# Kernel optimization log

Hardware: AMD Instinct MI355X
Metric: run time of the kernel (lower is better)

Reference implementation:

```python
import jax, jax.numpy as jnp
import numpy as np

EPS = 1e-5
P = 8  # patch size


def ln_chan(x, w, b):
    # LayerNorm over channel dim C of (B,C,H,W): per-pixel mean/var across channels
    mu = x.mean(axis=1, keepdims=True)
    var = x.var(axis=1, keepdims=True)
    return (x - mu) / jnp.sqrt(var + EPS) * w[None, :, None, None] + b[None, :, None, None]


def conv1x1(x, w):
    # w: (O, C) -> pointwise conv
    return jnp.einsum('bchw,oc->bohw', x, w)


def dwconv3(x, w):
    # depthwise 3x3, SAME padding; w: (C,1,3,3)
    return jax.lax.conv_general_dilated(
        x, w, window_strides=(1, 1), padding='SAME',
        dimension_numbers=('NCHW', 'OIHW', 'NCHW'),
        feature_group_count=x.shape[1])


def to_patches(t):
    b, c, h, w = t.shape
    return t.reshape(b, c, h // P, P, w // P, P).transpose(0, 1, 2, 4, 3, 5)


def from_patches(t, h, w):
    b, c = t.shape[:2]
    return t.transpose(0, 1, 2, 4, 3, 5).reshape(b, c, h, w)


def setup_inputs() -> dict:
    key = jax.random.key(0)
    ks = jax.random.split(key, 8)
    B, C, H, W = 4, 64, 256, 256
    s = 0.1  # weight scale to keep activations sane
    inp = {
        'x': jax.random.normal(ks[0], (B, C, H, W), jnp.float32),
        'evt': jax.random.normal(ks[1], (B, C, H, W), jnp.float32),
        'w_q': jax.random.normal(ks[2], (2 * C, C), jnp.float32) * s,
        'w_kv': jax.random.normal(ks[3], (4 * C, C), jnp.float32) * s,
        'w_qdw': jax.random.normal(ks[4], (2 * C, 1, 3, 3), jnp.float32) * s,
        'w_kvdw': jax.random.normal(ks[5], (4 * C, 1, 3, 3), jnp.float32) * s,
        'w_proj': jax.random.normal(ks[6], (C, 2 * C), jnp.float32) * s,
        'ln_img_w': jnp.ones((C,), jnp.float32),
        'ln_img_b': jnp.zeros((C,), jnp.float32),
        'ln_evt_w': jnp.ones((C,), jnp.float32),
        'ln_evt_b': jnp.zeros((C,), jnp.float32),
        'ln_out_w': jnp.ones((2 * C,), jnp.float32),
        'ln_out_b': jnp.zeros((2 * C,), jnp.float32),
    }
    return inp


def reference(x, evt, w_q, w_kv, w_qdw, w_kvdw, w_proj,
              ln_img_w, ln_img_b, ln_evt_w, ln_evt_b, ln_out_w, ln_out_b):
    x = ln_chan(x, ln_img_w, ln_img_b)
    evt = ln_chan(evt, ln_evt_w, ln_evt_b)
    q = dwconv3(conv1x1(x, w_q), w_qdw)          # (B, 2C, H, W)
    kv = dwconv3(conv1x1(evt, w_kv), w_kvdw)     # (B, 4C, H, W)
    k, v = jnp.split(kv, 2, axis=1)
    h, w = q.shape[-2:]
    q_fft = jnp.fft.rfft2(to_patches(q))         # (B,2C,h/8,w/8,8,5) complex
    k_fft = jnp.fft.rfft2(to_patches(k))
    out = jnp.fft.irfft2(q_fft * k_fft, s=(P, P))
    out = from_patches(out, h, w)                # (B, 2C, H, W)
    out = ln_chan(out, ln_out_w, ln_out_b)
    out = v * out
    return conv1x1(out, w_proj)                  # (B, C, H, W)
```

## Files before the change

### kernel.cpp

```cpp
#include <hip/hip_runtime.h>

typedef __attribute__((ext_vector_type(8))) short bf16x8;
typedef __attribute__((ext_vector_type(4))) float f32x4;
typedef __attribute__((ext_vector_type(2))) float f32x2;
typedef __attribute__((ext_vector_type(4))) unsigned int u32x4;
typedef __attribute__((ext_vector_type(2))) unsigned int u32x2;

__device__ __forceinline__ unsigned short f2bf(float f) {
    union { float f; unsigned int u; } v; v.f = f;
    return (unsigned short)((v.u + 0x7fffu + ((v.u >> 16) & 1u)) >> 16);
}
__device__ __forceinline__ float bflo(unsigned int u) {
    union { unsigned int u; float f; } v; v.u = u << 16; return v.f;
}
__device__ __forceinline__ float bfhi(unsigned int u) {
    union { unsigned int u; float f; } v; v.u = u & 0xffff0000u; return v.f;
}
__device__ __forceinline__ f32x2 bfpair(unsigned int u) {
    union { unsigned int u; float f; } lo, hi;
    lo.u = u << 16; hi.u = u & 0xffff0000u;
    return (f32x2){lo.f, hi.f};
}
__device__ __forceinline__ void pkfma(f32x2& d, f32x2 a, f32x2 b) {
    asm("v_pk_fma_f32 %0, %1, %2, %0" : "+v"(d) : "v"(a), "v"(b));
}

__device__ __forceinline__ float wred_allsum(float x) {
    asm volatile(
        "s_nop 1\n\t"
        "v_add_f32_dpp %0, %0, %0 row_shr:1 bound_ctrl:0\n\t"
        "s_nop 1\n\t"
        "v_add_f32_dpp %0, %0, %0 row_shr:2 bound_ctrl:0\n\t"
        "s_nop 1\n\t"
        "v_add_f32_dpp %0, %0, %0 row_shr:4 bound_ctrl:0\n\t"
        "s_nop 1\n\t"
        "v_add_f32_dpp %0, %0, %0 row_shr:8 bound_ctrl:0\n\t"
        "s_nop 1\n\t"
        "v_add_f32_dpp %0, %0, %0 row_bcast:15 row_mask:0xa bound_ctrl:0\n\t"
        "s_nop 1\n\t"
        "v_add_f32_dpp %0, %0, %0 row_bcast:31 row_mask:0xc bound_ctrl:0\n\t"
        "s_nop 1"
        : "+v"(x));
    return __builtin_bit_cast(float, __builtin_amdgcn_readlane(__builtin_bit_cast(int, x), 63));
}

__global__ __launch_bounds__(256, 8)
void ln_kernel(const float* __restrict__ x, const float* __restrict__ evt,
               const float* __restrict__ lwx, const float* __restrict__ lbx,
               const float* __restrict__ lwe, const float* __restrict__ lbe,
               unsigned short* __restrict__ xo, unsigned short* __restrict__ eo)
{
    __shared__ float xt[64][68];
    __shared__ float ps[4][64], ps2[4][64];
    __shared__ float smu[64], sinv[64], slw[64], slb[64];

    const int tid = threadIdx.x;
    const int z = blockIdx.z, b = blockIdx.y;
    const int hw0 = blockIdx.x * 64;
    const float* src = z ? evt : x;
    const float* lw  = z ? lwe : lwx;
    const float* lb  = z ? lbe : lbx;
    unsigned short* dst = z ? eo : xo;

    if (tid < 64) { slw[tid] = lw[tid]; slb[tid] = lb[tid]; }

    const float* sp = src + (size_t)b * 64 * 65536 + hw0;
    #pragma unroll
    for (int it = 0; it < 4; ++it) {
        int i = tid + it * 256;
        int c = i >> 4, p4 = i & 15;
        f32x4 v = *(const f32x4*)&sp[(size_t)c * 65536 + p4 * 4];
        xt[p4 * 4 + 0][c] = v.x;
        xt[p4 * 4 + 1][c] = v.y;
        xt[p4 * 4 + 2][c] = v.z;
        xt[p4 * 4 + 3][c] = v.w;
    }
    __syncthreads();

    {
        int px = tid & 63, part = tid >> 6;
        float s = 0.f, s2 = 0.f;
        #pragma unroll
        for (int j = 0; j < 4; ++j) {
            f32x4 v = *(const f32x4*)&xt[px][part * 16 + j * 4];
            s  += v.x + v.y + v.z + v.w;
            s2 += v.x * v.x + v.y * v.y + v.z * v.z + v.w * v.w;
        }
        ps[part][px] = s; ps2[part][px] = s2;
    }
    __syncthreads();
    if (tid < 64) {
        float s  = ps[0][tid] + ps[1][tid] + ps[2][tid] + ps[3][tid];
        float s2 = ps2[0][tid] + ps2[1][tid] + ps2[2][tid] + ps2[3][tid];
        float mu = s * (1.f / 64.f);
        smu[tid] = mu;
        sinv[tid] = rsqrtf(s2 * (1.f / 64.f) - mu * mu + 1e-5f);
    }
    __syncthreads();

    unsigned short* dp = dst + ((size_t)b * 65536 + hw0) * 64;
    #pragma unroll
    for (int it = 0; it < 2; ++it) {
        int i = tid + it * 256;
        int px = i >> 3, oct = i & 7;
        float mu = smu[px], inv = sinv[px];
        f32x4 v0 = *(const f32x4*)&xt[px][oct * 8];
        f32x4 v1 = *(const f32x4*)&xt[px][oct * 8 + 4];
        u32x4 w;
        int c = oct * 8;
        float a0 = (v0.x - mu) * inv * slw[c + 0] + slb[c + 0];
        float a1 = (v0.y - mu) * inv * slw[c + 1] + slb[c + 1];
        w[0] = (unsigned int)f2bf(a0) | ((unsigned int)f2bf(a1) << 16);
        a0 = (v0.z - mu) * inv * slw[c + 2] + slb[c + 2];
        a1 = (v0.w - mu) * inv * slw[c + 3] + slb[c + 3];
        w[1] = (unsigned int)f2bf(a0) | ((unsigned int)f2bf(a1) << 16);
        a0 = (v1.x - mu) * inv * slw[c + 4] + slb[c + 4];
        a1 = (v1.y - mu) * inv * slw[c + 5] + slb[c + 5];
        w[2] = (unsigned int)f2bf(a0) | ((unsigned int)f2bf(a1) << 16);
        a0 = (v1.z - mu) * inv * slw[c + 6] + slb[c + 6];
        a1 = (v1.w - mu) * inv * slw[c + 7] + slb[c + 7];
        w[3] = (unsigned int)f2bf(a0) | ((unsigned int)f2bf(a1) << 16);
        *(u32x4*)&dp[(size_t)px * 64 + oct * 8] = w;
    }
}

#define PR_WB    14336
#define PR_WDW   30720
#define PR_SMEM  35328

__global__ __launch_bounds__(512, 8)
void prod_kernel(const unsigned short* __restrict__ src,
                 const float* __restrict__ wmat, const float* __restrict__ wdw,
                 unsigned short* __restrict__ dst)
{
    __shared__ __align__(16) char smem[PR_SMEM];
    unsigned short* A   = (unsigned short*)(smem);
    unsigned short* Wb  = (unsigned short*)(smem + PR_WB);
    unsigned short* pre = (unsigned short*)(smem);
    float* swdw = (float*)(smem + PR_WDW);

    const int tid = threadIdx.x;
    const int pj = blockIdx.x, pi = blockIdx.y, b = blockIdx.z;
    const int h0 = pi * 8, w0 = pj * 8;

    #pragma unroll
    for (int it = 0; it < 4; ++it) {
        int i = tid + it * 512;
        int o = i >> 4, c4 = i & 15;
        f32x4 wv = *(const f32x4*)&wmat[o * 64 + c4 * 4];
        unsigned int lo = (unsigned int)f2bf(wv[0]) | ((unsigned int)f2bf(wv[1]) << 16);
        unsigned int hi = (unsigned int)f2bf(wv[2]) | ((unsigned int)f2bf(wv[3]) << 16);
        u32x2 pk = {lo, hi};
        *(u32x2*)&Wb[o * 64 + (((c4 >> 1) ^ (o & 7)) << 3) + (c4 & 1) * 4] = pk;
    }
    for (int i = tid; i < 1152; i += 512) swdw[i] = wdw[i];
    for (int i = tid; i < 768; i += 512) A[6400 + i] = 0;
    #pragma unroll
    for (int it = 0; it < 2; ++it) {
        int i = tid + it * 512;
        if (i < 800) {
            int px = i >> 3, oct = i & 7;
            int r = px / 10, cc = px - r * 10;
            int gh = h0 - 1 + r, gw = w0 - 1 + cc;
            u32x4 val = {0u, 0u, 0u, 0u};
            if (gh >= 0 && gh < 256 && gw >= 0 && gw < 256)
                val = *(const u32x4*)&src[((size_t)(b * 65536 + gh * 256 + gw)) * 64 + oct * 8];
            *(u32x4*)&A[px * 64 + ((oct ^ (px & 7)) << 3)] = val;
        }
    }
    __syncthreads();

    const int lane = tid & 63;
    const int l15 = lane & 15, l4 = lane >> 4;
    const int o_n = (tid >> 6) * 16 + l15;
    f32x4 acc[7];
    #pragma unroll
    for (int mt = 0; mt < 7; ++mt) acc[mt] = (f32x4){0.f, 0.f, 0.f, 0.f};
    #pragma unroll
    for (int ks = 0; ks < 2; ++ks) {
        int cch = ks * 4 + l4;
        bf16x8 bfrag = *(const bf16x8*)&Wb[o_n * 64 + ((cch ^ (o_n & 7)) << 3)];
        #pragma unroll
        for (int mt = 0; mt < 7; ++mt) {
            int px = mt * 16 + l15;
            bf16x8 afrag = *(const bf16x8*)&A[px * 64 + ((cch ^ (px & 7)) << 3)];
            acc[mt] = __builtin_amdgcn_mfma_f32_16x16x32_bf16(afrag, bfrag, acc[mt], 0, 0, 0);
        }
    }
    __syncthreads();

    #pragma unroll
    for (int mt = 0; mt < 7; ++mt)
        #pragma unroll
        for (int r = 0; r < 4; ++r) {
            int px = mt * 16 + l4 * 4 + r;
            if (px < 100)
                pre[px * 128 + (((o_n >> 3) ^ (px & 7)) << 3) + (o_n & 7)] = f2bf(acc[mt][r]);
        }
    __syncthreads();

    f32x2 res[8];
    {
        const int o = (tid & 63) * 2;
        const int och = o >> 3, osub = o & 7;
        const int pc = tid >> 6;
        f32x2 wdp[9];
        #pragma unroll
        for (int t = 0; t < 9; ++t)
            wdp[t] = (f32x2){swdw[o * 9 + t], swdw[o * 9 + 9 + t]};

        f32x2 ra[3], rb[3], rc[3];
        #define LOADROW(dstv, rr)                                                        \
            {                                                                            \
                _Pragma("unroll")                                                        \
                for (int d = 0; d < 3; ++d) {                                            \
                    int hp = (rr) * 10 + pc + d;                                         \
                    unsigned int u = *(const unsigned int*)                              \
                        &pre[hp * 128 + ((och ^ (hp & 7)) << 3) + osub];                 \
                    dstv[d] = bfpair(u);                                                 \
                }                                                                        \
            }
        LOADROW(ra, 0)
        LOADROW(rb, 1)
        #pragma unroll
        for (int r = 2; r < 10; ++r) {
            LOADROW(rc, r)
            f32x2 s = ra[0] * wdp[0];
            s += ra[1] * wdp[1]; s += ra[2] * wdp[2];
            s += rb[0] * wdp[3]; s += rb[1] * wdp[4]; s += rb[2] * wdp[5];
            s += rc[0] * wdp[6]; s += rc[1] * wdp[7]; s += rc[2] * wdp[8];
            res[r - 2] = s;
            #pragma unroll
            for (int d = 0; d < 3; ++d) { ra[d] = rb[d]; rb[d] = rc[d]; }
        }
        #undef LOADROW
    }
    __syncthreads();

    {
        unsigned short* ldout = (unsigned short*)smem;
        const int o = (tid & 63) * 2;
        const int pc = tid >> 6;
        const int key = pc << 4;
        #pragma unroll
        for (int r = 0; r < 8; ++r) {
            int px = r * 8 + pc;
            unsigned int pk = (unsigned int)f2bf(res[r].x) | ((unsigned int)f2bf(res[r].y) << 16);
            *(unsigned int*)&ldout[px * 128 + (o ^ key)] = pk;
        }
    }
    __syncthreads();

    {
        unsigned short* ldout = (unsigned short*)smem;
        const int c0 = (tid & 63) * 2;
        const int s = tid >> 6;
        const int sl = s ^ (tid & 7);
        const size_t patchbase = ((size_t)(b * 32 + pi) * 32 + pj) * 8192;
        unsigned int rv[8];
        #pragma unroll
        for (int j = 0; j < 8; ++j)
            rv[j] = *(const unsigned int*)&ldout[(8 * s + j) * 128 + (c0 ^ (j << 4))];
        u32x4 lo, hi;
        #pragma unroll
        for (int d = 0; d < 4; ++d) {
            lo[d] = (rv[2 * d] & 0xffffu) | (rv[2 * d + 1] << 16);
            hi[d] = (rv[2 * d] >> 16) | (rv[2 * d + 1] & 0xffff0000u);
        }
        *(u32x4*)&dst[patchbase + (size_t)c0 * 64 + sl * 8]       = lo;
        *(u32x4*)&dst[patchbase + (size_t)(c0 + 1) * 64 + sl * 8] = hi;
    }
}

#define PK_Q    0
#define PK_K    16384
#define PK_WP   32768
#define PK_LW   49152
#define PK_LB   49664
#define PK_SMEM 50176

__global__ __launch_bounds__(512, 6)
void patch_kernel(const unsigned short* __restrict__ qb,
                  const unsigned short* __restrict__ kb,
                  const unsigned short* __restrict__ vb,
                  const float* __restrict__ w_proj,
                  const float* __restrict__ lnw, const float* __restrict__ lnb,
                  float* __restrict__ out)
{
    __shared__ __align__(16) char smem[PK_SMEM];
    unsigned short* sq  = (unsigned short*)(smem + PK_Q);
    unsigned short* sk  = (unsigned short*)(smem + PK_K);
    unsigned short* sy  = sq;
    float*          sc  = (float*)(smem + PK_K);
    unsigned short* swp = (unsigned short*)(smem + PK_WP);
    float* slw = (float*)(smem + PK_LW);
    float* slb = (float*)(smem + PK_LB);

    const int tid = threadIdx.x;
    const int tj = blockIdx.x, ti = blockIdx.y, b = blockIdx.z;
    const int h0 = ti * 8, w0 = tj * 8;
    const size_t pbase = ((size_t)(b * 32 + ti) * 32 + tj) * 8192;

    const int pr = tid >> 6;
    const int cq = tid & 63;
    const int key = cq & 7;

    u32x4 vreg0 = *(const u32x4*)&vb[pbase + (2 * cq) * 64 + ((pr ^ key) << 3)];
    u32x4 vreg1 = *(const u32x4*)&vb[pbase + (2 * cq + 1) * 64 + ((pr ^ key) << 3)];

    if (tid < 128) { slw[tid] = lnw[tid]; slb[tid] = lnb[tid]; }
    #pragma unroll
    for (int it = 0; it < 2; ++it) {
        int i = tid + it * 512;
        *(u32x4*)&sq[i * 8] = *(const u32x4*)&qb[pbase + i * 8];
        *(u32x4*)&sk[i * 8] = *(const u32x4*)&kb[pbase + i * 8];
    }
    #pragma unroll
    for (int it = 0; it < 4; ++it) {
        int i = tid + it * 512;
        int o = i >> 5, c4 = i & 31;
        f32x4 wv = *(const f32x4*)&w_proj[o * 128 + c4 * 4];
        unsigned int lo = (unsigned int)f2bf(wv[0]) | ((unsigned int)f2bf(wv[1]) << 16);
        unsigned int hi = (unsigned int)f2bf(wv[2]) | ((unsigned int)f2bf(wv[3]) << 16);
        u32x2 pk = {lo, hi};
        *(u32x2*)&swp[o * 128 + (((c4 >> 1) ^ (o & 7)) << 3) + (c4 & 1) * 4] = pk;
    }
    __syncthreads();

    const float lw0 = slw[2 * cq], lw1 = slw[2 * cq + 1];
    const float lb0 = slb[2 * cq], lb1 = slb[2 * cq + 1];

    f32x2 acc[8];
    #pragma unroll
    for (int pc = 0; pc < 8; ++pc) acc[pc] = (f32x2){0.f, 0.f};
    #pragma unroll
    for (int tr = 0; tr < 8; ++tr) {
        const int qs = (tr ^ key) << 3;
        u32x4 q0 = *(const u32x4*)&sq[(2 * cq) * 64 + qs];
        u32x4 q1 = *(const u32x4*)&sq[(2 * cq + 1) * 64 + qs];
        const int rrow = (pr - tr) & 7;
        const int ksl = (rrow ^ key) << 3;
        u32x4 k0 = *(const u32x4*)&sk[(2 * cq) * 64 + ksl];
        u32x4 k1 = *(const u32x4*)&sk[(2 * cq + 1) * 64 + ksl];
        f32x2 kp[8];
        #pragma unroll
        for (int d = 0; d < 4; ++d) {
            kp[2 * d]     = (f32x2){bflo(k0[d]), bflo(k1[d])};
            kp[2 * d + 1] = (f32x2){bfhi(k0[d]), bfhi(k1[d])};
        }
        #pragma unroll
        for (int tc = 0; tc < 8; ++tc) {
            const int d = tc >> 1;
            f32x2 qp = (tc & 1) ? (f32x2){bfhi(q0[d]), bfhi(q1[d])}
                                : (f32x2){bflo(q0[d]), bflo(q1[d])};
            #pragma unroll
            for (int pc = 0; pc < 8; ++pc)
                pkfma(acc[pc], qp, kp[(pc - tc) & 7]);
        }
    }
    __syncthreads();

    float mu[8], inv[8];
    #pragma unroll
    for (int pc = 0; pc < 8; ++pc) {
        float s  = wred_allsum(acc[pc].x + acc[pc].y);
        float s2 = wred_allsum(acc[pc].x * acc[pc].x + acc[pc].y * acc[pc].y);
        float m_ = s * (1.f / 128.f);
        mu[pc]  = m_;
        inv[pc] = rsqrtf(s2 * (1.f / 128.f) - m_ * m_ + 1e-5f);
    }

    #pragma unroll
    for (int pc = 0; pc < 8; ++pc) {
        int px = pr * 8 + pc;
        const int d = pc >> 1;
        f32x2 vp = (pc & 1) ? (f32x2){bfhi(vreg0[d]), bfhi(vreg1[d])}
                            : (f32x2){bflo(vreg0[d]), bflo(vreg1[d])};
        float y0 = ((acc[pc].x - mu[pc]) * inv[pc] * lw0 + lb0) * vp.x;
        float y1 = ((acc[pc].y - mu[pc]) * inv[pc] * lw1 + lb1) * vp.y;
        unsigned int pk = (unsigned int)f2bf(y0) | ((unsigned int)f2bf(y1) << 16);
        *(unsigned int*)&sy[px * 128 + (((cq >> 2) ^ (px & 7)) << 3) + 2 * (cq & 3)] = pk;
    }
    __syncthreads();

    {
        const int lane = tid & 63;
        const int l15 = lane & 15, l4 = lane >> 4;
        const int wave = tid >> 6;
        const int mt = wave >> 1;
        const int nt0 = 2 * (wave & 1);
        f32x4 pacc[2];
        pacc[0] = (f32x4){0.f, 0.f, 0.f, 0.f};
        pacc[1] = (f32x4){0.f, 0.f, 0.f, 0.f};
        const int px_a = mt * 16 + l15;
        #pragma unroll
        for (int ks = 0; ks < 4; ++ks) {
            int cch = ks * 4 + l4;
            bf16x8 af = *(const bf16x8*)&sy[px_a * 128 + ((cch ^ (px_a & 7)) << 3)];
            #pragma unroll
            for (int p2 = 0; p2 < 2; ++p2) {
                int o_n = (nt0 + p2) * 16 + l15;
                bf16x8 bfr = *(const bf16x8*)&swp[o_n * 128 + ((cch ^ (o_n & 7)) << 3)];
                pacc[p2] = __builtin_amdgcn_mfma_f32_16x16x32_bf16(af, bfr, pacc[p2], 0, 0, 0);
            }
        }
        #pragma unroll
        for (int p2 = 0; p2 < 2; ++p2)
            #pragma unroll
            for (int r = 0; r < 4; ++r) {
                int px = mt * 16 + l4 * 4 + r;
                int o = (nt0 + p2) * 16 + l15;
                sc[px * 64 + o] = pacc[p2][r];
            }
    }
    __syncthreads();

    {
        const int o = tid & 63, r = tid >> 6;
        float v0[4], v1[4];
        #pragma unroll
        for (int j = 0; j < 4; ++j) {
            v0[j] = sc[(r * 8 + j) * 64 + o];
            v1[j] = sc[(r * 8 + 4 + j) * 64 + o];
        }
        int obase = ((b * 64 + o) * 256 + h0 + r) * 256 + w0;
        *(f32x4*)&out[obase]     = (f32x4){v0[0], v0[1], v0[2], v0[3]};
        *(f32x4*)&out[obase + 4] = (f32x4){v1[0], v1[1], v1[2], v1[3]};
    }
}

extern "C" void kernel_launch(void* const* d_in, const int* in_sizes, int n_in,
                              void* d_out, int out_size, void* d_ws, size_t ws_size,
                              hipStream_t stream) {
    (void)in_sizes; (void)n_in; (void)out_size; (void)ws_size;
    const float* x        = (const float*)d_in[0];
    const float* evt      = (const float*)d_in[1];
    const float* w_q      = (const float*)d_in[2];
    const float* w_kv     = (const float*)d_in[3];
    const float* w_qdw    = (const float*)d_in[4];
    const float* w_kvdw   = (const float*)d_in[5];
    const float* w_proj   = (const float*)d_in[6];
    const float* ln_img_w = (const float*)d_in[7];
    const float* ln_img_b = (const float*)d_in[8];
    const float* ln_evt_w = (const float*)d_in[9];
    const float* ln_evt_b = (const float*)d_in[10];
    const float* ln_out_w = (const float*)d_in[11];
    const float* ln_out_b = (const float*)d_in[12];
    float* out = (float*)d_out;

    const size_t NPATCH = (size_t)4 * 32 * 32 * 8192;
    const size_t NLN    = (size_t)4 * 65536 * 64;
    unsigned short* qd  = (unsigned short*)d_ws;
    unsigned short* kd  = qd + NPATCH;
    unsigned short* eln = kd + NPATCH;
    unsigned short* xln = eln + NLN;
    unsigned short* vd  = xln;

    dim3 lgrid(1024, 4, 2), lblk(256);
    ln_kernel<<<lgrid, lblk, 0, stream>>>(x, evt, ln_img_w, ln_img_b,
                                          ln_evt_w, ln_evt_b, xln, eln);
    dim3 grid(32, 32, 4), blk(512);
    prod_kernel<<<grid, blk, 0, stream>>>(xln, w_q,            w_qdw,           qd);
    prod_kernel<<<grid, blk, 0, stream>>>(eln, w_kv,           w_kvdw,          kd);
    prod_kernel<<<grid, blk, 0, stream>>>(eln, w_kv + 128*64,  w_kvdw + 128*9,  vd);
    patch_kernel<<<grid, blk, 0, stream>>>(qd, kd, vd, w_proj, ln_out_w, ln_out_b, out);
}
```

Before: 282.4 us.

## Compute patch circular convolution via MFMA DFT matmuls instead of direct FMA

Replaces the direct 8x8 circular convolution per channel, done with packed FP32 FMAs, with a 64-point 2D DFT expressed as bf16 MFMA matmuls against an in-LDS twiddle table. The pointwise complex product is taken and the inverse is applied as another MFMA matmul. This moves the dominant arithmetic onto matrix cores but adds bf16 rounding of the twiddles and spectra, more LDS (66KB, occupancy hint lowered from 6 to 4) and extra barriers. It also changes the swizzle of the producer's output layout so the transposed loads line up.

```diff
diff --git a/kernel.cpp b/kernel.cpp
--- a/kernel.cpp
+++ b/kernel.cpp
@@ -21,8 +21,14 @@
     lo.u = u << 16; hi.u = u & 0xffff0000u;
     return (f32x2){lo.f, hi.f};
 }
-__device__ __forceinline__ void pkfma(f32x2& d, f32x2 a, f32x2 b) {
-    asm("v_pk_fma_f32 %0, %1, %2, %0" : "+v"(d) : "v"(a), "v"(b));
+
+__device__ __forceinline__ unsigned short costab(int m) {
+    unsigned short mag = (m & 1) ? 0x3F35 : (((m & 3) == 0) ? 0x3F80 : 0);
+    return mag | (((m >= 3) && (m <= 5)) ? 0x8000 : 0);
+}
+__device__ __forceinline__ unsigned short nsintab(int m) {
+    unsigned short mag = (m & 1) ? 0x3F35 : (((m & 3) == 2) ? 0x3F80 : 0);
+    return mag | (((m >= 1) && (m <= 3)) ? 0x8000 : 0);
 }
 
 __device__ __forceinline__ float wred_allsum(float x) {
@@ -255,7 +261,8 @@
         unsigned short* ldout = (unsigned short*)smem;
         const int c0 = (tid & 63) * 2;
         const int s = tid >> 6;
-        const int sl = s ^ (tid & 7);
+        const int sl0 = s ^ (c0 & 7);
+        const int sl1 = s ^ ((c0 + 1) & 7);
         const size_t patchbase = ((size_t)(b * 32 + pi) * 32 + pj) * 8192;
         unsigned int rv[8];
         #pragma unroll
@@ -267,19 +274,20 @@
             lo[d] = (rv[2 * d] & 0xffffu) | (rv[2 * d + 1] << 16);
             hi[d] = (rv[2 * d] >> 16) | (rv[2 * d + 1] & 0xffff0000u);
         }
-        *(u32x4*)&dst[patchbase + (size_t)c0 * 64 + sl * 8]       = lo;
-        *(u32x4*)&dst[patchbase + (size_t)(c0 + 1) * 64 + sl * 8] = hi;
-    }
-}
-
-#define PK_Q    0
-#define PK_K    16384
-#define PK_WP   32768
-#define PK_LW   49152
-#define PK_LB   49664
-#define PK_SMEM 50176
-
-__global__ __launch_bounds__(512, 6)
+        *(u32x4*)&dst[patchbase + (size_t)c0 * 64 + sl0 * 8]       = lo;
+        *(u32x4*)&dst[patchbase + (size_t)(c0 + 1) * 64 + sl1 * 8] = hi;
+    }
+}
+
+#define PK_R0   0
+#define PK_R1   16384
+#define PK_F    32768
+#define PK_WP   49152
+#define PK_LW   65536
+#define PK_LB   66048
+#define PK_SMEM 66560
+
+__global__ __launch_bounds__(512, 4)
 void patch_kernel(const unsigned short* __restrict__ qb,
                   const unsigned short* __restrict__ kb,
                   const unsigned short* __restrict__ vb,
@@ -288,11 +296,16 @@
                   float* __restrict__ out)
 {
     __shared__ __align__(16) char smem[PK_SMEM];
-    unsigned short* sq  = (unsigned short*)(smem + PK_Q);
-    unsigned short* sk  = (unsigned short*)(smem + PK_K);
-    unsigned short* sy  = sq;
-    float*          sc  = (float*)(smem + PK_K);
-    unsigned short* swp = (unsigned short*)(smem + PK_WP);
+    unsigned short* sqT  = (unsigned short*)(smem + PK_R0);
+    unsigned short* skT  = (unsigned short*)(smem + PK_R1);
+    unsigned short* ohr  = sqT;
+    unsigned short* ohi  = skT;
+    float*          out2 = (float*)smem;
+    unsigned short* sFre = (unsigned short*)(smem + PK_F);
+    unsigned short* sFim = (unsigned short*)(smem + PK_F + 8192);
+    unsigned short* swp  = (unsigned short*)(smem + PK_WP);
+    unsigned short* sy   = (unsigned short*)(smem + PK_R1);
+    float*          sc   = (float*)(smem + PK_R0);
     float* slw = (float*)(smem + PK_LW);
     float* slb = (float*)(smem + PK_LB);
 
@@ -303,17 +316,16 @@
 
     const int pr = tid >> 6;
     const int cq = tid & 63;
-    const int key = cq & 7;
-
-    u32x4 vreg0 = *(const u32x4*)&vb[pbase + (2 * cq) * 64 + ((pr ^ key) << 3)];
-    u32x4 vreg1 = *(const u32x4*)&vb[pbase + (2 * cq + 1) * 64 + ((pr ^ key) << 3)];
+
+    u32x4 vreg0 = *(const u32x4*)&vb[pbase + (2 * cq) * 64 + ((pr ^ ((2 * cq) & 7)) << 3)];
+    u32x4 vreg1 = *(const u32x4*)&vb[pbase + (2 * cq + 1) * 64 + ((pr ^ ((2 * cq + 1) & 7)) << 3)];
 
     if (tid < 128) { slw[tid] = lnw[tid]; slb[tid] = lnb[tid]; }
     #pragma unroll
     for (int it = 0; it < 2; ++it) {
         int i = tid + it * 512;
-        *(u32x4*)&sq[i * 8] = *(const u32x4*)&qb[pbase + i * 8];
-        *(u32x4*)&sk[i * 8] = *(const u32x4*)&kb[pbase + i * 8];
+        *(u32x4*)&sqT[i * 8] = *(const u32x4*)&qb[pbase + i * 8];
+        *(u32x4*)&skT[i * 8] = *(const u32x4*)&kb[pbase + i * 8];
     }
     #pragma unroll
     for (int it = 0; it < 4; ++it) {
@@ -325,41 +337,114 @@
         u32x2 pk = {lo, hi};
         *(u32x2*)&swp[o * 128 + (((c4 >> 1) ^ (o & 7)) << 3) + (c4 & 1) * 4] = pk;
     }
+    #pragma unroll
+    for (int it = 0; it < 8; ++it) {
+        int i = tid + it * 512;
+        int f = i >> 6, t = i & 63;
+        int m = ((f >> 3) * (t >> 3) + (f & 7) * (t & 7)) & 7;
+        int pos = f * 64 + ((((t >> 3) ^ (f & 7)) << 3)) + (t & 7);
+        sFre[pos] = costab(m);
+        sFim[pos] = nsintab(m);
+    }
+    __syncthreads();
+
+    const int lane = tid & 63;
+    const int l15 = lane & 15, l4 = lane >> 4;
+    const int wid = tid >> 6;
+    const int ntile = wid >> 1;
+    const int mtbase = (wid & 1) * 4;
+    const int fcol = ntile * 16 + l15;
+
+    bf16x8 bre[2], bim[2];
+    #pragma unroll
+    for (int ks = 0; ks < 2; ++ks) {
+        int cch = ks * 4 + l4;
+        int off = fcol * 64 + ((cch ^ (fcol & 7)) << 3);
+        bre[ks] = *(const bf16x8*)&sFre[off];
+        bim[ks] = *(const bf16x8*)&sFim[off];
+    }
+    f32x4 fr_[4], fi_[4];
+    #pragma unroll
+    for (int mt = 0; mt < 4; ++mt) {
+        const int crow = (mtbase + mt) * 16 + l15;
+        bf16x8 aq[2], ak[2];
+        #pragma unroll
+        for (int ks = 0; ks < 2; ++ks) {
+            int cch = ks * 4 + l4;
+            int off = crow * 64 + ((cch ^ (crow & 7)) << 3);
+            aq[ks] = *(const bf16x8*)&sqT[off];
+            ak[ks] = *(const bf16x8*)&skT[off];
+        }
+        f32x4 qr = {0.f,0.f,0.f,0.f}, qi = qr, kr = qr, ki = qr;
+        qr = __builtin_amdgcn_mfma_f32_16x16x32_bf16(aq[0], bre[0], qr, 0, 0, 0);
+        qr = __builtin_amdgcn_mfma_f32_16x16x32_bf16(aq[1], bre[1], qr, 0, 0, 0);
+        qi = __builtin_amdgcn_mfma_f32_16x16x32_bf16(aq[0], bim[0], qi, 0, 0, 0);
+        qi = __builtin_amdgcn_mfma_f32_16x16x32_bf16(aq[1], bim[1], qi, 0, 0, 0);
+        kr = __builtin_amdgcn_mfma_f32_16x16x32_bf16(ak[0], bre[0], kr, 0, 0, 0);
+        kr = __builtin_amdgcn_mfma_f32_16x16x32_bf16(ak[1], bre[1], kr, 0, 0, 0);
+        ki = __builtin_amdgcn_mfma_f32_16x16x32_bf16(ak[0], bim[0], ki, 0, 0, 0);
+        ki = __builtin_amdgcn_mfma_f32_16x16x32_bf16(ak[1], bim[1], ki, 0, 0, 0);
+        fr_[mt] = (qr * kr - qi * ki) * 0.015625f;
+        fi_[mt] = (qr * ki + qi * kr) * 0.015625f;
+    }
+    __syncthreads();
+
+    #pragma unroll
+    for (int mt = 0; mt < 4; ++mt)
+        #pragma unroll
+        for (int r = 0; r < 4; ++r) {
+            int c = (mtbase + mt) * 16 + l4 * 4 + r;
+            int pos = c * 64 + (((fcol >> 3) ^ (c & 7)) << 3) + (fcol & 7);
+            ohr[pos] = f2bf(fr_[mt][r]);
+            ohi[pos] = f2bf(fi_[mt][r]);
+        }
+    __syncthreads();
+
+    const int prow = ntile * 16 + l15;
+    bf16x8 gre[2], gim[2];
+    #pragma unroll
+    for (int ks = 0; ks < 2; ++ks) {
+        int cch = ks * 4 + l4;
+        int off = prow * 64 + ((cch ^ (prow & 7)) << 3);
+        gre[ks] = *(const bf16x8*)&sFre[off];
+        gim[ks] = *(const bf16x8*)&sFim[off];
+    }
+    f32x4 oreg[4];
+    #pragma unroll
+    for (int mt = 0; mt < 4; ++mt) {
+        const int crow = (mtbase + mt) * 16 + l15;
+        bf16x8 ar[2], ai[2];
+        #pragma unroll
+        for (int ks = 0; ks < 2; ++ks) {
+            int cch = ks * 4 + l4;
+            int off = crow * 64 + ((cch ^ (crow & 7)) << 3);
+            ar[ks] = *(const bf16x8*)&ohr[off];
+            ai[ks] = *(const bf16x8*)&ohi[off];
+        }
+        f32x4 o2 = {0.f,0.f,0.f,0.f};
+        o2 = __builtin_amdgcn_mfma_f32_16x16x32_bf16(ar[0], gre[0], o2, 0, 0, 0);
+        o2 = __builtin_amdgcn_mfma_f32_16x16x32_bf16(ar[1], gre[1], o2, 0, 0, 0);
+        o2 = __builtin_amdgcn_mfma_f32_16x16x32_bf16(ai[0], gim[0], o2, 0, 0, 0);
+        o2 = __builtin_amdgcn_mfma_f32_16x16x32_bf16(ai[1], gim[1], o2, 0, 0, 0);
+        oreg[mt] = o2;
+    }
+    __syncthreads();
+
+    #pragma unroll
+    for (int mt = 0; mt < 4; ++mt) {
+        int c0 = (mtbase + mt) * 16 + l4 * 4;
+        *(f32x4*)&out2[prow * 128 + (c0 ^ ((prow & 7) << 2))] = oreg[mt];
+    }
     __syncthreads();
 
     const float lw0 = slw[2 * cq], lw1 = slw[2 * cq + 1];
     const float lb0 = slb[2 * cq], lb1 = slb[2 * cq + 1];
-
     f32x2 acc[8];
     #pragma unroll
-    for (int pc = 0; pc < 8; ++pc) acc[pc] = (f32x2){0.f, 0.f};
-    #pragma unroll
-    for (int tr = 0; tr < 8; ++tr) {
-        const int qs = (tr ^ key) << 3;
-        u32x4 q0 = *(const u32x4*)&sq[(2 * cq) * 64 + qs];
-        u32x4 q1 = *(const u32x4*)&sq[(2 * cq + 1) * 64 + qs];
-        const int rrow = (pr - tr) & 7;
-        const int ksl = (rrow ^ key) << 3;
-        u32x4 k0 = *(const u32x4*)&sk[(2 * cq) * 64 + ksl];
-        u32x4 k1 = *(const u32x4*)&sk[(2 * cq + 1) * 64 + ksl];
-        f32x2 kp[8];
-        #pragma unroll
-        for (int d = 0; d < 4; ++d) {
-            kp[2 * d]     = (f32x2){bflo(k0[d]), bflo(k1[d])};
-            kp[2 * d + 1] = (f32x2){bfhi(k0[d]), bfhi(k1[d])};
-        }
-        #pragma unroll
-        for (int tc = 0; tc < 8; ++tc) {
-            const int d = tc >> 1;
-            f32x2 qp = (tc & 1) ? (f32x2){bfhi(q0[d]), bfhi(q1[d])}
-                                : (f32x2){bflo(q0[d]), bflo(q1[d])};
-            #pragma unroll
-            for (int pc = 0; pc < 8; ++pc)
-                pkfma(acc[pc], qp, kp[(pc - tc) & 7]);
-        }
-    }
-    __syncthreads();
-
+    for (int pc = 0; pc < 8; ++pc) {
+        int px = pr * 8 + pc;
+        acc[pc] = *(const f32x2*)&out2[px * 128 + ((2 * cq) ^ ((px & 7) << 2))];
+    }
     float mu[8], inv[8];
     #pragma unroll
     for (int pc = 0; pc < 8; ++pc) {
@@ -369,6 +454,7 @@
         mu[pc]  = m_;
         inv[pc] = rsqrtf(s2 * (1.f / 128.f) - m_ * m_ + 1e-5f);
     }
+    __syncthreads();
 
     #pragma unroll
     for (int pc = 0; pc < 8; ++pc) {
@@ -384,11 +470,8 @@
     __syncthreads();
 
     {
-        const int lane = tid & 63;
-        const int l15 = lane & 15, l4 = lane >> 4;
-        const int wave = tid >> 6;
-        const int mt = wave >> 1;
-        const int nt0 = 2 * (wave & 1);
+        const int mt = wid >> 1;
+        const int nt0 = 2 * (wid & 1);
         f32x4 pacc[2];
         pacc[0] = (f32x4){0.f, 0.f, 0.f, 0.f};
         pacc[1] = (f32x4){0.f, 0.f, 0.f, 0.f};
```

After: 282.7 us. No clear change (+0.1%).
